# Optimization experiments

Measured on AMD Instinct MI355X. Metric: run time of the kernel, lower is better.

## Reference

```python
import jax, jax.numpy as jnp
import numpy as np

B, T, N, E = 8, 16, 2048, 32768
F_IN, C, EDGE_DIM = 32, 32, 1


def setup_inputs() -> dict:
    key = jax.random.key(0)
    ks = jax.random.split(key, 12)
    s = 1.0 / np.sqrt(C)
    x = jax.random.normal(ks[0], (B, T, N, F_IN), jnp.float32)
    edge_index = jax.random.randint(ks[1], (2, E), 0, N)
    edge_attr = jax.random.normal(ks[2], (E, EDGE_DIM), jnp.float32)
    Wl = jax.random.normal(ks[3], (F_IN, C), jnp.float32) * s
    bl = jnp.zeros((C,), jnp.float32)
    Wr = jax.random.normal(ks[4], (F_IN, C), jnp.float32) * s
    br = jnp.zeros((C,), jnp.float32)
    We = jax.random.normal(ks[5], (EDGE_DIM, C), jnp.float32) * s
    att = jax.random.normal(ks[6], (C,), jnp.float32) * s
    out_bias = jnp.zeros((C,), jnp.float32)
    w_ih = jax.random.normal(ks[7], (3 * C, C), jnp.float32) * s
    w_hh = jax.random.normal(ks[8], (3 * C, C), jnp.float32) * s
    b_ih = jnp.zeros((3 * C,), jnp.float32)
    b_hh = jnp.zeros((3 * C,), jnp.float32)
    return dict(x=x, edge_index=edge_index, edge_attr=edge_attr, Wl=Wl, bl=bl,
                Wr=Wr, br=br, We=We, att=att, out_bias=out_bias,
                w_ih=w_ih, w_hh=w_hh, b_ih=b_ih, b_hh=b_hh)


def _gatv2(x, edge_index, edge_attr, Wl, bl, Wr, br, We, att, out_bias):
    # x: [B,T,N,F]; GATv2Conv, heads=1, negative_slope=0.2, self loops w/ mean edge attr
    n = x.shape[2]
    src, dst = edge_index[0], edge_index[1]
    deg = jax.ops.segment_sum(jnp.ones((src.shape[0],), x.dtype), dst, num_segments=n)
    mean_attr = jax.ops.segment_sum(edge_attr, dst, num_segments=n) / jnp.maximum(deg, 1.0)[:, None]
    loop = jnp.arange(n)
    src_a = jnp.concatenate([src, loop])
    dst_a = jnp.concatenate([dst, loop])
    attr_a = jnp.concatenate([edge_attr, mean_attr], axis=0)
    xl = x @ Wl + bl  # [B,T,N,C]
    xr = x @ Wr + br
    e_emb = attr_a @ We  # [E2,C]
    xls = jnp.take(xl, src_a, axis=2)  # [B,T,E2,C]
    m = jax.nn.leaky_relu(xls + jnp.take(xr, dst_a, axis=2) + e_emb, 0.2)
    s = jnp.einsum('btec,c->ebt', m, att)  # [E2,B,T]
    smax = jax.ops.segment_max(s, dst_a, num_segments=n)
    es = jnp.exp(s - smax[dst_a])
    denom = jax.ops.segment_sum(es, dst_a, num_segments=n)
    alpha = es / denom[dst_a]  # segment softmax over incoming edges, [E2,B,T]
    msg = xls * alpha.transpose(1, 2, 0)[..., None]  # [B,T,E2,C]
    out = jax.ops.segment_sum(msg.transpose(2, 0, 1, 3), dst_a, num_segments=n)
    return out.transpose(1, 2, 0, 3) + out_bias  # [B,T,N,C]


def _gru(seq, w_ih, w_hh, b_ih, b_hh):
    # seq: [BN, T, C]; torch GRU gate order r,z,n
    c = seq.shape[-1]

    def step(h, xt):
        gi = xt @ w_ih.T + b_ih
        gh = h @ w_hh.T + b_hh
        ir, iz, inn = jnp.split(gi, 3, axis=-1)
        hr, hz, hn = jnp.split(gh, 3, axis=-1)
        r = jax.nn.sigmoid(ir + hr)
        z = jax.nn.sigmoid(iz + hz)
        nc = jnp.tanh(inn + r * hn)
        h = (1.0 - z) * nc + z * h
        return h, h

    h0 = jnp.zeros((seq.shape[0], c), seq.dtype)
    _, ys = jax.lax.scan(step, h0, seq.transpose(1, 0, 2))
    return ys.transpose(1, 0, 2)


def reference(x, edge_index, edge_attr, Wl, bl, Wr, br, We, att, out_bias, w_ih, w_hh, b_ih, b_hh):
    b, t, n, _ = x.shape
    h = _gatv2(x, edge_index, edge_attr, Wl, bl, Wr, br, We, att, out_bias)
    seq = h.transpose(0, 2, 1, 3).reshape(b * n, t, -1)
    y = _gru(seq, w_ih, w_hh, b_ih, b_hh)
    return y.reshape(b, n, t, -1).transpose(0, 2, 1, 3)
```

## Files before the change

kernel.cpp:

```cpp
#include <hip/hip_runtime.h>

#define N_NODES 2048
#define N_EDGES 32768
#define BT      128
#define TT      16
#define CH      32
#define E2      (N_EDGES + N_NODES)

__global__ void deg_attr_kernel(const int* __restrict__ ei,
                                const float* __restrict__ ea,
                                int* __restrict__ deg, float* __restrict__ asum) {
    int e = blockIdx.x * 256 + threadIdx.x;
    if (e < N_EDGES) {
        int dst = ei[N_EDGES + e];
        atomicAdd(&deg[dst], 1);
        atomicAdd(&asum[dst], ea[e]);
    }
}

__global__ void scan_kernel(const int* __restrict__ deg, int* __restrict__ rowp) {
    int lane = threadIdx.x;
    int base = lane * 32;
    int loc[32];
    int s = 0;
    #pragma unroll
    for (int i = 0; i < 32; ++i) { loc[i] = s; s += deg[base + i] + 1; }
    int inc = s;
    #pragma unroll
    for (int d = 1; d < 64; d <<= 1) {
        int v = __shfl_up(inc, d, 64);
        if (lane >= d) inc += v;
    }
    int excl = inc - s;
    #pragma unroll
    for (int i = 0; i < 32; ++i) rowp[base + i] = excl + loc[i];
    if (lane == 63) rowp[N_NODES] = inc;
}

__global__ void scatter_kernel(const int* __restrict__ ei,
                               const float* __restrict__ ea,
                               const int* __restrict__ deg, const float* __restrict__ asum,
                               const int* __restrict__ rowp, int* __restrict__ fill,
                               int* __restrict__ col, float* __restrict__ attr_s) {
    int e = blockIdx.x * 256 + threadIdx.x;
    if (e >= E2) return;
    int src, dst; float a;
    if (e < N_EDGES) {
        src = ei[e]; dst = ei[N_EDGES + e]; a = ea[e];
    } else {
        int n = e - N_EDGES;
        src = n; dst = n;
        a = asum[n] / fmaxf((float)deg[n], 1.0f);
    }
    int pos = atomicAdd(&fill[dst], 1);
    col[rowp[dst] + pos]    = src;
    attr_s[rowp[dst] + pos] = a;
}

__global__ __launch_bounds__(256) void proj_kernel(
        const float* __restrict__ x,
        const float* __restrict__ Wl, const float* __restrict__ bl,
        const float* __restrict__ Wr, const float* __restrict__ br,
        float* __restrict__ xlt, float* __restrict__ xr) {
    __shared__ float xs[128 * 32];
    __shared__ float wl[1024], wr[1024];
    int n = blockIdx.x;
    int tid = threadIdx.x;
    for (int i = tid; i < 1024; i += 256) { wl[i] = Wl[i]; wr[i] = Wr[i]; }
    #pragma unroll
    for (int i = 0; i < 16; ++i) {
        int e = i * 256 + tid;
        int bt = e >> 5, f = e & 31;
        xs[e] = x[((long)bt * N_NODES + n) * 32 + f];
    }
    __syncthreads();
    int c = tid & 31;
    int btl = tid >> 5;
    float blc = bl[c], brc = br[c];
    for (int i = 0; i < 16; ++i) {
        int bt = i * 8 + btl;
        float al = 0.f, ar = 0.f;
        #pragma unroll
        for (int f = 0; f < 32; ++f) {
            float xv = xs[bt * 32 + f];
            al += xv * wl[f * 32 + c];
            ar += xv * wr[f * 32 + c];
        }
        xlt[((long)n * 32 + c) * 128 + bt]   = al + blc;
        xr[((long)bt * N_NODES + n) * 32 + c] = ar + brc;
    }
}

__global__ __launch_bounds__(256) void gat_kernel(
        const float* __restrict__ xlt,
        const float* __restrict__ xr,
        const int* __restrict__ rowp, const int* __restrict__ col,
        const float* __restrict__ attr_s,
        const float* __restrict__ We, const float* __restrict__ att,
        const float* __restrict__ ob,
        float* __restrict__ out) {
    int tid = threadIdx.x;
    int wv = tid >> 6, lane = tid & 63;
    int task = blockIdx.x * 4 + wv;
    int n   = task >> 1;
    int bt  = ((task & 1) << 6) | lane;

    float Wec[32], attc[32];
    #pragma unroll
    for (int c = 0; c < 32; ++c) { Wec[c] = We[c]; attc[c] = att[c]; }

    float xrv[32], accv[32];
    const float* xrp = xr + ((long)bt * N_NODES + n) * CH;
    #pragma unroll
    for (int c = 0; c < 32; ++c) { xrv[c] = xrp[c]; accv[c] = 0.f; }

    int beg = rowp[n];
    int end = rowp[n + 1];
    float den = 0.f;
    const float* xbase = xlt + bt;
    for (int j = beg; j < end; ++j) {
        int   src = col[j];
        float av  = attr_s[j];
        const float* gp = xbase + (long)src * (CH * 128);
        float xlv[32];
        #pragma unroll
        for (int c = 0; c < 32; ++c) xlv[c] = gp[c * 128];
        float p0 = 0.f, p1 = 0.f, p2 = 0.f, p3 = 0.f;
        #pragma unroll
        for (int k = 0; k < 8; ++k) {
            { int c = k;      float m = xlv[c] + fmaf(av, Wec[c], xrv[c]); p0 = fmaf(attc[c], fmaxf(m, 0.2f * m), p0); }
            { int c = k + 8;  float m = xlv[c] + fmaf(av, Wec[c], xrv[c]); p1 = fmaf(attc[c], fmaxf(m, 0.2f * m), p1); }
            { int c = k + 16; float m = xlv[c] + fmaf(av, Wec[c], xrv[c]); p2 = fmaf(attc[c], fmaxf(m, 0.2f * m), p2); }
            { int c = k + 24; float m = xlv[c] + fmaf(av, Wec[c], xrv[c]); p3 = fmaf(attc[c], fmaxf(m, 0.2f * m), p3); }
        }
        float p = fminf((p0 + p1) + (p2 + p3), 80.f);
        float w = __expf(p);
        den += w;
        #pragma unroll
        for (int c = 0; c < 32; ++c) accv[c] = fmaf(w, xlv[c], accv[c]);
    }
    float inv = 1.f / den;
    float* op = out + ((long)bt * N_NODES + n) * CH;
    #pragma unroll
    for (int c = 0; c < 32; ++c) op[c] = fmaf(accv[c], inv, ob[c]);
}

__global__ __launch_bounds__(256, 2) void gru_kernel(
        const float* __restrict__ wih, const float* __restrict__ whh,
        const float* __restrict__ bih, const float* __restrict__ bhh,
        float* __restrict__ hio) {
    int tid  = threadIdx.x;
    int lane = tid & 63;
    int c    = lane & 31;
    int half = lane >> 5;
    int sbase = lane & 32;
    int seq  = blockIdx.x * 4 + (tid >> 6);
    int b = seq >> 11;
    int n = seq & 2047;

    const float* W  = half ? whh : wih;
    const float* Bs = half ? bhh : bih;
    float w0[32], w1[32], w2[32];
    #pragma unroll
    for (int f4 = 0; f4 < 8; ++f4) {
        float4 a0 = *(const float4*)&W[( 0 + c) * 32 + f4 * 4];
        float4 a1 = *(const float4*)&W[(32 + c) * 32 + f4 * 4];
        float4 a2 = *(const float4*)&W[(64 + c) * 32 + f4 * 4];
        w0[f4*4+0]=a0.x; w0[f4*4+1]=a0.y; w0[f4*4+2]=a0.z; w0[f4*4+3]=a0.w;
        w1[f4*4+0]=a1.x; w1[f4*4+1]=a1.y; w1[f4*4+2]=a1.z; w1[f4*4+3]=a1.w;
        w2[f4*4+0]=a2.x; w2[f4*4+1]=a2.y; w2[f4*4+2]=a2.z; w2[f4*4+3]=a2.w;
    }
    #pragma unroll
    for (int f = 0; f < 32; ++f) {
        asm volatile("" : "+v"(w0[f]), "+v"(w1[f]), "+v"(w2[f]));
    }
    float b0 = Bs[c], b1 = Bs[32 + c], b2 = Bs[64 + c];

    const long STR = (long)N_NODES * CH;
    long base = ((long)b * TT) * STR + (long)n * CH + c;

    float hc = 0.f;
    float xv = hio[base];
    #pragma unroll 1
    for (int t = 0; t < TT; ++t) {
        float xnext = (t + 1 < TT) ? hio[base + (long)(t + 1) * STR] : 0.f;
        float src = half ? hc : xv;
        float g0 = b0, g1 = b1, g2 = b2;
        #pragma unroll
        for (int f = 0; f < 32; ++f) {
            float v = __shfl(src, sbase | f, 64);
            g0 = fmaf(v, w0[f], g0);
            g1 = fmaf(v, w1[f], g1);
            g2 = fmaf(v, w2[f], g2);
        }
        float p0 = g0 + __shfl_xor(g0, 32, 64);
        float p1 = g1 + __shfl_xor(g1, 32, 64);
        float q2 = __shfl_xor(g2, 32, 64);
        float gx2 = half ? q2 : g2;
        float gh2 = half ? g2 : q2;
        float r  = 1.f / (1.f + __expf(-p0));
        float z  = 1.f / (1.f + __expf(-p1));
        float a  = fmaf(r, gh2, gx2);
        float e2 = __expf(2.f * a);
        float nc = 1.f - 2.f / (e2 + 1.f);
        hc = (1.f - z) * nc + z * hc;
        if (half == 0) hio[base + (long)t * STR] = hc;
        xv = xnext;
    }
}

extern "C" void kernel_launch(void* const* d_in, const int* in_sizes, int n_in,
                              void* d_out, int out_size, void* d_ws, size_t ws_size,
                              hipStream_t stream) {
    const float* x    = (const float*)d_in[0];
    const int*   ei   = (const int*)d_in[1];
    const float* ea   = (const float*)d_in[2];
    const float* Wl   = (const float*)d_in[3];
    const float* bl   = (const float*)d_in[4];
    const float* Wr   = (const float*)d_in[5];
    const float* br   = (const float*)d_in[6];
    const float* We   = (const float*)d_in[7];
    const float* att  = (const float*)d_in[8];
    const float* ob   = (const float*)d_in[9];
    const float* wih  = (const float*)d_in[10];
    const float* whh  = (const float*)d_in[11];
    const float* bih  = (const float*)d_in[12];
    const float* bhh  = (const float*)d_in[13];
    float* out = (float*)d_out;

    const long RB = (long)BT * N_NODES * CH;
    int*   deg  = (int*)d_ws;
    float* asum = (float*)(deg + N_NODES);
    int*   fill = (int*)(asum + N_NODES);
    int*   rowp = fill + N_NODES;
    int*   col  = rowp + (N_NODES + 16);
    float* attr_s = (float*)(col + E2);
    float* xlt  = (float*)(attr_s + E2);
    xlt = (float*)(((uintptr_t)xlt + 255) & ~(uintptr_t)255);
    float* xr   = xlt + RB;

    hipMemsetAsync(deg, 0, 3 * N_NODES * sizeof(int), stream);

    deg_attr_kernel<<<N_EDGES / 256, 256, 0, stream>>>(ei, ea, deg, asum);
    scan_kernel<<<1, 64, 0, stream>>>(deg, rowp);
    scatter_kernel<<<(E2 + 255) / 256, 256, 0, stream>>>(ei, ea, deg, asum, rowp, fill, col, attr_s);
    proj_kernel<<<N_NODES, 256, 0, stream>>>(x, Wl, bl, Wr, br, xlt, xr);
    gat_kernel<<<(N_NODES * 2) / 4, 256, 0, stream>>>(xlt, xr, rowp, col, attr_s, We, att, ob, out);
    gru_kernel<<<(BT / TT * N_NODES) / 4, 256, 0, stream>>>(wih, whh, bih, bhh, out);
}
```

Baseline: 274.9 us.

## Fuse Wr projection and GRU input transform into GAT kernel

Result: faster. 257.9 us (-6.2%).

```diff
diff --git a/kernel.cpp b/kernel.cpp
--- a/kernel.cpp
+++ b/kernel.cpp
@@ -60,13 +60,12 @@
 __global__ __launch_bounds__(256) void proj_kernel(
         const float* __restrict__ x,
         const float* __restrict__ Wl, const float* __restrict__ bl,
-        const float* __restrict__ Wr, const float* __restrict__ br,
-        float* __restrict__ xlt, float* __restrict__ xr) {
+        float* __restrict__ xlt) {
     __shared__ float xs[128 * 32];
-    __shared__ float wl[1024], wr[1024];
+    __shared__ float wl[1024];
     int n = blockIdx.x;
     int tid = threadIdx.x;
-    for (int i = tid; i < 1024; i += 256) { wl[i] = Wl[i]; wr[i] = Wr[i]; }
+    for (int i = tid; i < 1024; i += 256) wl[i] = Wl[i];
     #pragma unroll
     for (int i = 0; i < 16; ++i) {
         int e = i * 256 + tid;
@@ -76,43 +75,54 @@
     __syncthreads();
     int c = tid & 31;
     int btl = tid >> 5;
-    float blc = bl[c], brc = br[c];
+    float blc = bl[c];
     for (int i = 0; i < 16; ++i) {
         int bt = i * 8 + btl;
-        float al = 0.f, ar = 0.f;
-        #pragma unroll
-        for (int f = 0; f < 32; ++f) {
-            float xv = xs[bt * 32 + f];
-            al += xv * wl[f * 32 + c];
-            ar += xv * wr[f * 32 + c];
-        }
-        xlt[((long)n * 32 + c) * 128 + bt]   = al + blc;
-        xr[((long)bt * N_NODES + n) * 32 + c] = ar + brc;
+        float al = 0.f;
+        #pragma unroll
+        for (int f = 0; f < 32; ++f)
+            al = fmaf(xs[bt * 32 + f], wl[f * 32 + c], al);
+        xlt[((long)n * 32 + c) * 128 + bt] = al + blc;
     }
 }
 
 __global__ __launch_bounds__(256) void gat_kernel(
         const float* __restrict__ xlt,
-        const float* __restrict__ xr,
+        const float* __restrict__ x,
         const int* __restrict__ rowp, const int* __restrict__ col,
         const float* __restrict__ attr_s,
+        const float* __restrict__ Wr, const float* __restrict__ br,
         const float* __restrict__ We, const float* __restrict__ att,
         const float* __restrict__ ob,
-        float* __restrict__ out) {
+        const float* __restrict__ wih, const float* __restrict__ bih,
+        float* __restrict__ gi) {
     int tid = threadIdx.x;
     int wv = tid >> 6, lane = tid & 63;
     int task = blockIdx.x * 4 + wv;
     int n   = task >> 1;
     int bt  = ((task & 1) << 6) | lane;
 
-    float Wec[32], attc[32];
-    #pragma unroll
-    for (int c = 0; c < 32; ++c) { Wec[c] = We[c]; attc[c] = att[c]; }
-
-    float xrv[32], accv[32];
-    const float* xrp = xr + ((long)bt * N_NODES + n) * CH;
-    #pragma unroll
-    for (int c = 0; c < 32; ++c) { xrv[c] = xrp[c]; accv[c] = 0.f; }
+    float xf[32];
+    {
+        const float* xp = x + ((long)bt * N_NODES + n) * 32;
+        #pragma unroll
+        for (int f4 = 0; f4 < 8; ++f4) {
+            float4 a = *(const float4*)(xp + f4 * 4);
+            xf[f4*4+0]=a.x; xf[f4*4+1]=a.y; xf[f4*4+2]=a.z; xf[f4*4+3]=a.w;
+        }
+    }
+    float xrv[32];
+    #pragma unroll
+    for (int c = 0; c < 32; ++c) {
+        float s = br[c];
+        #pragma unroll
+        for (int f = 0; f < 32; ++f) s = fmaf(xf[f], Wr[f * 32 + c], s);
+        xrv[c] = s;
+    }
+
+    float accv[32];
+    #pragma unroll
+    for (int c = 0; c < 32; ++c) accv[c] = 0.f;
 
     int beg = rowp[n];
     int end = rowp[n + 1];
@@ -128,10 +138,10 @@
         float p0 = 0.f, p1 = 0.f, p2 = 0.f, p3 = 0.f;
         #pragma unroll
         for (int k = 0; k < 8; ++k) {
-            { int c = k;      float m = xlv[c] + fmaf(av, Wec[c], xrv[c]); p0 = fmaf(attc[c], fmaxf(m, 0.2f * m), p0); }
-            { int c = k + 8;  float m = xlv[c] + fmaf(av, Wec[c], xrv[c]); p1 = fmaf(attc[c], fmaxf(m, 0.2f * m), p1); }
-            { int c = k + 16; float m = xlv[c] + fmaf(av, Wec[c], xrv[c]); p2 = fmaf(attc[c], fmaxf(m, 0.2f * m), p2); }
-            { int c = k + 24; float m = xlv[c] + fmaf(av, Wec[c], xrv[c]); p3 = fmaf(attc[c], fmaxf(m, 0.2f * m), p3); }
+            { int c = k;      float m = xlv[c] + fmaf(av, We[c], xrv[c]); p0 = fmaf(att[c], fmaxf(m, 0.2f * m), p0); }
+            { int c = k + 8;  float m = xlv[c] + fmaf(av, We[c], xrv[c]); p1 = fmaf(att[c], fmaxf(m, 0.2f * m), p1); }
+            { int c = k + 16; float m = xlv[c] + fmaf(av, We[c], xrv[c]); p2 = fmaf(att[c], fmaxf(m, 0.2f * m), p2); }
+            { int c = k + 24; float m = xlv[c] + fmaf(av, We[c], xrv[c]); p3 = fmaf(att[c], fmaxf(m, 0.2f * m), p3); }
         }
         float p = fminf((p0 + p1) + (p2 + p3), 80.f);
         float w = __expf(p);
@@ -140,72 +150,84 @@
         for (int c = 0; c < 32; ++c) accv[c] = fmaf(w, xlv[c], accv[c]);
     }
     float inv = 1.f / den;
-    float* op = out + ((long)bt * N_NODES + n) * CH;
-    #pragma unroll
-    for (int c = 0; c < 32; ++c) op[c] = fmaf(accv[c], inv, ob[c]);
-}
-
-__global__ __launch_bounds__(256, 2) void gru_kernel(
-        const float* __restrict__ wih, const float* __restrict__ whh,
-        const float* __restrict__ bih, const float* __restrict__ bhh,
-        float* __restrict__ hio) {
+    #pragma unroll
+    for (int c = 0; c < 32; ++c) accv[c] = fmaf(accv[c], inv, ob[c]);
+
+    float* gip = gi + ((long)bt * N_NODES + n) * 96;
+    #pragma unroll
+    for (int g4 = 0; g4 < 24; ++g4) {
+        float s0 = bih[g4*4+0], s1 = bih[g4*4+1], s2 = bih[g4*4+2], s3 = bih[g4*4+3];
+        #pragma unroll
+        for (int f = 0; f < 32; ++f) {
+            float hf = accv[f];
+            s0 = fmaf(hf, wih[(g4*4+0)*32+f], s0);
+            s1 = fmaf(hf, wih[(g4*4+1)*32+f], s1);
+            s2 = fmaf(hf, wih[(g4*4+2)*32+f], s2);
+            s3 = fmaf(hf, wih[(g4*4+3)*32+f], s3);
+        }
+        float4 v = make_float4(s0, s1, s2, s3);
+        *(float4*)(gip + g4*4) = v;
+    }
+}
+
+__global__ __launch_bounds__(256) void gru_kernel(
+        const float* __restrict__ whh, const float* __restrict__ bhh,
+        const float* __restrict__ gi,
+        float* __restrict__ out) {
     int tid  = threadIdx.x;
     int lane = tid & 63;
     int c    = lane & 31;
     int half = lane >> 5;
-    int sbase = lane & 32;
+    int fbase = half << 4;
     int seq  = blockIdx.x * 4 + (tid >> 6);
     int b = seq >> 11;
     int n = seq & 2047;
 
-    const float* W  = half ? whh : wih;
-    const float* Bs = half ? bhh : bih;
-    float w0[32], w1[32], w2[32];
-    #pragma unroll
-    for (int f4 = 0; f4 < 8; ++f4) {
-        float4 a0 = *(const float4*)&W[( 0 + c) * 32 + f4 * 4];
-        float4 a1 = *(const float4*)&W[(32 + c) * 32 + f4 * 4];
-        float4 a2 = *(const float4*)&W[(64 + c) * 32 + f4 * 4];
-        w0[f4*4+0]=a0.x; w0[f4*4+1]=a0.y; w0[f4*4+2]=a0.z; w0[f4*4+3]=a0.w;
-        w1[f4*4+0]=a1.x; w1[f4*4+1]=a1.y; w1[f4*4+2]=a1.z; w1[f4*4+3]=a1.w;
-        w2[f4*4+0]=a2.x; w2[f4*4+1]=a2.y; w2[f4*4+2]=a2.z; w2[f4*4+3]=a2.w;
-    }
-    #pragma unroll
-    for (int f = 0; f < 32; ++f) {
-        asm volatile("" : "+v"(w0[f]), "+v"(w1[f]), "+v"(w2[f]));
-    }
-    float b0 = Bs[c], b1 = Bs[32 + c], b2 = Bs[64 + c];
-
-    const long STR = (long)N_NODES * CH;
-    long base = ((long)b * TT) * STR + (long)n * CH + c;
+    float w0[16], w1[16], w2[16];
+    #pragma unroll
+    for (int k4 = 0; k4 < 4; ++k4) {
+        float4 a0 = *(const float4*)&whh[( 0 + c) * 32 + fbase + k4 * 4];
+        float4 a1 = *(const float4*)&whh[(32 + c) * 32 + fbase + k4 * 4];
+        float4 a2 = *(const float4*)&whh[(64 + c) * 32 + fbase + k4 * 4];
+        w0[k4*4+0]=a0.x; w0[k4*4+1]=a0.y; w0[k4*4+2]=a0.z; w0[k4*4+3]=a0.w;
+        w1[k4*4+0]=a1.x; w1[k4*4+1]=a1.y; w1[k4*4+2]=a1.z; w1[k4*4+3]=a1.w;
+        w2[k4*4+0]=a2.x; w2[k4*4+1]=a2.y; w2[k4*4+2]=a2.z; w2[k4*4+3]=a2.w;
+    }
+    float bh0 = half ? 0.f : bhh[c];
+    float bh1 = half ? 0.f : bhh[32 + c];
+    float bh2 = half ? 0.f : bhh[64 + c];
+
+    const long GSTR = (long)N_NODES * 96;
+    long gbase = ((long)b * TT * N_NODES + n) * 96 + c;
+    const long OSTR = (long)N_NODES * CH;
+    long obase = ((long)b * TT * N_NODES + n) * CH + c;
 
     float hc = 0.f;
-    float xv = hio[base];
+    float gr = gi[gbase], gz = gi[gbase + 32], gn = gi[gbase + 64];
     #pragma unroll 1
     for (int t = 0; t < TT; ++t) {
-        float xnext = (t + 1 < TT) ? hio[base + (long)(t + 1) * STR] : 0.f;
-        float src = half ? hc : xv;
-        float g0 = b0, g1 = b1, g2 = b2;
-        #pragma unroll
-        for (int f = 0; f < 32; ++f) {
-            float v = __shfl(src, sbase | f, 64);
-            g0 = fmaf(v, w0[f], g0);
-            g1 = fmaf(v, w1[f], g1);
-            g2 = fmaf(v, w2[f], g2);
-        }
-        float p0 = g0 + __shfl_xor(g0, 32, 64);
-        float p1 = g1 + __shfl_xor(g1, 32, 64);
-        float q2 = __shfl_xor(g2, 32, 64);
-        float gx2 = half ? q2 : g2;
-        float gh2 = half ? g2 : q2;
-        float r  = 1.f / (1.f + __expf(-p0));
-        float z  = 1.f / (1.f + __expf(-p1));
-        float a  = fmaf(r, gh2, gx2);
+        long gnx = gbase + (long)(t + 1) * GSTR;
+        float grn = 0.f, gzn = 0.f, gnn = 0.f;
+        if (t + 1 < TT) { grn = gi[gnx]; gzn = gi[gnx + 32]; gnn = gi[gnx + 64]; }
+        float g0 = bh0, g1 = bh1, g2 = bh2;
+        #pragma unroll
+        for (int k = 0; k < 16; ++k) {
+            float v = __shfl(hc, fbase + k, 64);
+            g0 = fmaf(v, w0[k], g0);
+            g1 = fmaf(v, w1[k], g1);
+            g2 = fmaf(v, w2[k], g2);
+        }
+        float G0 = g0 + __shfl_xor(g0, 32, 64);
+        float G1 = g1 + __shfl_xor(g1, 32, 64);
+        float G2 = g2 + __shfl_xor(g2, 32, 64);
+        float r  = 1.f / (1.f + __expf(-(gr + G0)));
+        float z  = 1.f / (1.f + __expf(-(gz + G1)));
+        float a  = fmaf(r, G2, gn);
         float e2 = __expf(2.f * a);
         float nc = 1.f - 2.f / (e2 + 1.f);
         hc = (1.f - z) * nc + z * hc;
-        if (half == 0) hio[base + (long)t * STR] = hc;
-        xv = xnext;
+        if (half == 0) out[obase + (long)t * OSTR] = hc;
+        gr = grn; gz = gzn; gn = gnn;
     }
 }
 
@@ -237,14 +259,15 @@
     float* attr_s = (float*)(col + E2);
     float* xlt  = (float*)(attr_s + E2);
     xlt = (float*)(((uintptr_t)xlt + 255) & ~(uintptr_t)255);
-    float* xr   = xlt + RB;
+    float* gi   = xlt + RB;
 
     hipMemsetAsync(deg, 0, 3 * N_NODES * sizeof(int), stream);
 
     deg_attr_kernel<<<N_EDGES / 256, 256, 0, stream>>>(ei, ea, deg, asum);
     scan_kernel<<<1, 64, 0, stream>>>(deg, rowp);
     scatter_kernel<<<(E2 + 255) / 256, 256, 0, stream>>>(ei, ea, deg, asum, rowp, fill, col, attr_s);
-    proj_kernel<<<N_NODES, 256, 0, stream>>>(x, Wl, bl, Wr, br, xlt, xr);
-    gat_kernel<<<(N_NODES * 2) / 4, 256, 0, stream>>>(xlt, xr, rowp, col, attr_s, We, att, ob, out);
-    gru_kernel<<<(BT / TT * N_NODES) / 4, 256, 0, stream>>>(wih, whh, bih, bhh, out);
-}
+    proj_kernel<<<N_NODES, 256, 0, stream>>>(x, Wl, bl, xlt);
+    gat_kernel<<<(N_NODES * 2) / 4, 256, 0, stream>>>(xlt, x, rowp, col, attr_s,
+                                                      Wr, br, We, att, ob, wih, bih, gi);
+    gru_kernel<<<(BT / TT * N_NODES) / 4, 256, 0, stream>>>(whh, bhh, gi, out);
+}
```
